# Performance work log

Hardware: AMD Instinct MI355X
Metric: run time of the kernel (lower is better)

Reference implementation:

```python
import jax, jax.numpy as jnp
import numpy as np

N = 100000
E = 1600000
IN_DIM = 128
OUT_DIM = 64


def setup_inputs() -> dict:
    key = jax.random.key(0)
    k_h, k_ei, k_ew, k_W, k_a = jax.random.split(key, 5)
    h = jax.random.normal(k_h, (N, IN_DIM), dtype=jnp.float32)
    edge_index = jax.random.randint(k_ei, (2, E), 0, N, dtype=jnp.int64)
    edge_weight = jax.random.uniform(k_ew, (E,), dtype=jnp.float32)
    # nn.Linear weights (Kaiming-uniform-ish scale)
    W = jax.random.uniform(k_W, (OUT_DIM, IN_DIM), dtype=jnp.float32,
                           minval=-1.0, maxval=1.0) / np.sqrt(IN_DIM)
    a = jax.random.uniform(k_a, (2 * OUT_DIM,), dtype=jnp.float32,
                           minval=-1.0, maxval=1.0) / np.sqrt(2 * OUT_DIM)
    return {"h": h, "edge_index": edge_index, "edge_weight": edge_weight,
            "W": W, "a": a}


def reference(h, edge_index, edge_weight, W, a):
    # Faithful translation of _GATConvSparse.forward (inference; dropout = identity).
    n = h.shape[0]
    src, dst = edge_index[0], edge_index[1]
    Wh = h @ W.T                                  # (N, out_dim)
    d = Wh.shape[1]
    # a(cat([Wh[src], Wh[dst]])) == Wh[src] @ a[:d] + Wh[dst] @ a[d:]
    alpha = Wh[src] @ a[:d] + Wh[dst] @ a[d:]     # (E,)
    alpha = alpha * edge_weight
    # Buggy-but-faithful 'softmax': segment-sum raw scores onto dst nodes...
    alpha_node = jax.ops.segment_sum(alpha, dst, num_segments=n)   # (N,)
    alpha_exp = jnp.exp(alpha_node - alpha_node.max())             # (N,)
    # ...then normalize per-edge exp(src) by sum of exp(src) over each dst segment.
    denom = jax.ops.segment_sum(alpha_exp[src], dst, num_segments=n)  # (N,)
    alpha_norm = alpha_exp[src] / (denom[dst] + 1e-9)              # (E,)
    out = jax.ops.segment_sum(alpha_norm[:, None] * Wh[src], dst,
                              num_segments=n)                      # (N, out_dim)
    return jax.nn.elu(out)
```

## Files before the change

kernel.cpp:

```cpp
#include <hip/hip_runtime.h>
#include <math.h>

#define Nn 100000
#define Ee 1600000
#define IND 128
#define OUTD 64
#define DPB 64
#define NB 1563
#define BSTR 1536
#define CAP 1536
#define GB 1563
#define EB_BLOCKS 391
#define AGG_BLOCKS 1024
#define AFIX 1048576.0f

using bf16x8 = __attribute__((ext_vector_type(8))) short;
using f32x4 = __attribute__((ext_vector_type(4))) float;

__device__ __forceinline__ unsigned short f2bf(float f) {
    unsigned u = __float_as_uint(f);
    u = u + 0x7FFFu + ((u >> 16) & 1u);
    return (unsigned short)(u >> 16);
}
__device__ __forceinline__ float bf2f(unsigned short h) {
    return __uint_as_float(((unsigned)h) << 16);
}

__device__ __forceinline__ bool probe64(const void* __restrict__ ei) {
    const long long* p = (const long long*)ei;
    bool ok = true;
#pragma unroll
    for (int i = 0; i < 8; ++i) {
        long long v = p[i];
        ok = ok && (v >= 0 && v < Nn);
    }
    return ok;
}

__device__ __forceinline__ void load_edge(const void* ei, int e, bool is64,
                                          int& s, int& d) {
    if (is64) {
        const long long* p = (const long long*)ei;
        s = (int)p[e];
        d = (int)p[Ee + e];
    } else {
        const int* p = (const int*)ei;
        s = p[e];
        d = p[Ee + e];
    }
}

__global__ __launch_bounds__(256) void k_fused(
    const float* __restrict__ h, const float* __restrict__ W,
    const float* __restrict__ a, unsigned short* __restrict__ Whb,
    float* __restrict__ s1, float* __restrict__ s2) {
    __shared__ unsigned short Ash[64][136];
    __shared__ unsigned short Wsh[64][136];
    __shared__ float al[2 * OUTD];
    int bid = blockIdx.x;
    int t = threadIdx.x;

    int R = bid * 64;
    for (int i = t; i < 2048; i += 256) {
        float4 v = ((const float4*)W)[i];
        int r = i >> 5, c = (i & 31) << 2;
        unsigned lo = (unsigned)f2bf(v.x) | ((unsigned)f2bf(v.y) << 16);
        unsigned hi = (unsigned)f2bf(v.z) | ((unsigned)f2bf(v.w) << 16);
        *(uint2*)&Wsh[r][c] = make_uint2(lo, hi);
    }
    if (t < 32) ((float4*)al)[t] = ((const float4*)a)[t];
    for (int i = t; i < 2048; i += 256) {
        int r = i >> 5, c = (i & 31) << 2;
        int n = R + r;
        float4 v = make_float4(0.f, 0.f, 0.f, 0.f);
        if (n < Nn) v = ((const float4*)(h + (size_t)n * IND))[i & 31];
        unsigned lo = (unsigned)f2bf(v.x) | ((unsigned)f2bf(v.y) << 16);
        unsigned hi = (unsigned)f2bf(v.z) | ((unsigned)f2bf(v.w) << 16);
        *(uint2*)&Ash[r][c] = make_uint2(lo, hi);
    }
    __syncthreads();

    int w = t >> 6, l = t & 63;
    int li = l & 15, lg = l >> 4;
    f32x4 acc[4];
#pragma unroll
    for (int nt = 0; nt < 4; ++nt) acc[nt] = (f32x4){0.f, 0.f, 0.f, 0.f};
#pragma unroll
    for (int kk = 0; kk < 4; ++kk) {
        bf16x8 af = *(const bf16x8*)&Ash[w * 16 + li][kk * 32 + lg * 8];
#pragma unroll
        for (int nt = 0; nt < 4; ++nt) {
            bf16x8 bf = *(const bf16x8*)&Wsh[nt * 16 + li][kk * 32 + lg * 8];
            acc[nt] = __builtin_amdgcn_mfma_f32_16x16x32_bf16(af, bf,
                                                              acc[nt],
                                                              0, 0, 0);
        }
    }
    float p1[4] = {0.f, 0.f, 0.f, 0.f};
    float p2[4] = {0.f, 0.f, 0.f, 0.f};
#pragma unroll
    for (int nt = 0; nt < 4; ++nt) {
        float a1v = al[nt * 16 + li];
        float a2v = al[OUTD + nt * 16 + li];
#pragma unroll
        for (int r = 0; r < 4; ++r) {
            float v = acc[nt][r];
            p1[r] += v * a1v;
            p2[r] += v * a2v;
            int row = R + w * 16 + lg * 4 + r;
            if (row < Nn)
                Whb[(size_t)row * OUTD + nt * 16 + li] = f2bf(v);
        }
    }
#pragma unroll
    for (int r = 0; r < 4; ++r) {
#pragma unroll
        for (int m = 1; m < 16; m <<= 1) {
            p1[r] += __shfl_xor(p1[r], m, 64);
            p2[r] += __shfl_xor(p2[r], m, 64);
        }
    }
    if (li < 4) {
        int row = R + w * 16 + lg * 4 + li;
        if (row < Nn) {
            s1[row] = p1[li];
            s2[row] = p2[li];
        }
    }
}

__global__ __launch_bounds__(512) void k_binscatter(
    const void* __restrict__ ei, const float* __restrict__ ew,
    const float* __restrict__ s1, const float* __restrict__ s2,
    int* __restrict__ bcursor, uint2* __restrict__ bins) {
    __shared__ int cnt[NB];
    __shared__ int gbase[NB];
    for (int i = threadIdx.x; i < NB; i += 512) cnt[i] = 0;
    __syncthreads();
    bool is64 = probe64(ei);
    int base = blockIdx.x * 4096;
    unsigned rx[8];
    int ryi[8];
    int rb[8];
    int rk[8];
#pragma unroll
    for (int i = 0; i < 8; ++i) {
        int e = base + i * 512 + threadIdx.x;
        rb[i] = -1;
        rx[i] = 0;
        ryi[i] = 0;
        rk[i] = 0;
        if (e < Ee) {
            int s, d;
            load_edge(ei, e, is64, s, d);
            float alpha = (s1[s] + s2[d]) * ew[e];
            ryi[i] = (int)rintf(alpha * AFIX);
            int b = d >> 6;
            rb[i] = b;
            rk[i] = atomicAdd(&cnt[b], 1);
            rx[i] = ((unsigned)s << 7) | ((unsigned)(d & 63) << 24);
        }
    }
    __syncthreads();
    for (int i = threadIdx.x; i < NB; i += 512) {
        int c = cnt[i];
        if (c) gbase[i] = atomicAdd(bcursor + i, c);
    }
    __syncthreads();
#pragma unroll
    for (int i = 0; i < 8; ++i) {
        if (rb[i] >= 0) {
            int pos = gbase[rb[i]] + rk[i];
            if (pos < BSTR)
                bins[(size_t)rb[i] * BSTR + pos] =
                    make_uint2(rx[i], (unsigned)ryi[i]);
        }
    }
}

__global__ __launch_bounds__(256) void k_balpha(
    const uint2* __restrict__ bins, const int* __restrict__ bcnt,
    float* __restrict__ ae) {
    __shared__ int anl[DPB];
    int b = blockIdx.x;
    int t = threadIdx.x;
    if (t < DPB) anl[t] = 0;
    __syncthreads();
    int e0 = b * BSTR;
    int c = bcnt[b];
    int e1 = e0 + (c < BSTR ? c : BSTR);
    for (int k = e0 + t; k < e1; k += 256) {
        uint2 r = bins[k];
        atomicAdd(&anl[r.x >> 24], (int)r.y);
    }
    __syncthreads();
    if (t < DPB) {
        int n = b * DPB + t;
        if (n < Nn) ae[n] = expf((float)anl[t] * (1.f / AFIX));
    }
}

#define AGG_BODY(NR)                                                         \
    {                                                                        \
        uint2 rr[NR];                                                        \
        uint2 ww[NR];                                                        \
        _Pragma("unroll") for (int j = 0; j < NR; ++j)                       \
            rr[j] = lp[4 * j];                                               \
        _Pragma("unroll") for (int j = 0; j < NR; ++j)                       \
            ww[j] = *(const uint2*)(whbB + (rr[j].x + ql8));                 \
        _Pragma("unroll") for (int j = 0; j < NR; ++j) {                     \
            float aa = __uint_as_float(rr[j].y);                             \
            acc.x += aa * __uint_as_float(ww[j].x << 16);                    \
            acc.y += aa * __uint_as_float(ww[j].x & 0xFFFF0000u);            \
            acc.z += aa * __uint_as_float(ww[j].y << 16);                    \
            acc.w += aa * __uint_as_float(ww[j].y & 0xFFFF0000u);            \
            den += aa;                                                       \
        }                                                                    \
        lp += 4 * NR;                                                        \
    }

__global__ __launch_bounds__(512, 4) void k_agg(
    const uint2* __restrict__ bins, const int* __restrict__ bcnt,
    const float* __restrict__ ae, const unsigned short* __restrict__ Whb,
    float* __restrict__ out, int* __restrict__ wctr) {
    __shared__ uint2 lrec[CAP];
    __shared__ int cnt[DPB];
    __shared__ int sbase[DPB];
    __shared__ int bsh;
    int t = threadIdx.x;
    int lane = t & 63;
    int wave = t >> 6;
    int q = lane >> 4;
    int ql = lane & 15;
    unsigned ql8 = (unsigned)ql << 3;
    const char* whbB = (const char*)Whb;

    for (;;) {
        if (t == 0) bsh = atomicAdd(wctr, 1);
        if (t < DPB) cnt[t] = 0;
        __syncthreads();
        int b = bsh;
        if (b >= NB) break;
        int e0 = b * BSTR;
        int c = bcnt[b];
        int total = c < BSTR ? c : BSTR;
        int e1 = e0 + total;

        unsigned su[CAP / 512];
        float sa[CAP / 512];
        int srk[CAP / 512];
#pragma unroll
        for (int i = 0; i < CAP / 512; ++i) {
            int k = e0 + i * 512 + t;
            srk[i] = -1;
            if (k < e1) {
                uint2 r = bins[k];
                srk[i] = atomicAdd(&cnt[r.x >> 24], 1);
                su[i] = r.x;
                sa[i] = ae[(r.x >> 7) & 0x1FFFF];
            }
        }
        __syncthreads();
        if (t < DPB) {
            int v = cnt[t];
#pragma unroll
            for (int d = 1; d < DPB; d <<= 1) {
                int u = __shfl_up(v, d, 64);
                if (t >= d) v += u;
            }
            sbase[t] = v;
        }
        __syncthreads();
#pragma unroll
        for (int i = 0; i < CAP / 512; ++i) {
            if (srk[i] >= 0) {
                int dloc = su[i] >> 24;
                int pos = sbase[dloc] - cnt[dloc] + srk[i];
                lrec[pos] = make_uint2(su[i] & 0x00FFFF80u,
                                       __float_as_uint(sa[i]));
            }
        }
        __syncthreads();

        for (int d = wave * 8; d < wave * 8 + 8; ++d) {
            int k1 = sbase[d];
            int k = k1 - cnt[d];
            const uint2* lp = lrec + k + q;
            float4 acc = make_float4(0.f, 0.f, 0.f, 0.f);
            float den = 0.f;
            for (; k + 15 < k1; k += 16) AGG_BODY(4);
            for (; k + 7 < k1; k += 8) AGG_BODY(2);
            for (; k + 3 < k1; k += 4) AGG_BODY(1);
            if (k < k1) {
                int idx = k + q;
                int cl = idx < k1 ? idx : k1 - 1;
                uint2 rA = lrec[cl];
                float aA = idx < k1 ? __uint_as_float(rA.y) : 0.f;
                uint2 wA = *(const uint2*)(whbB + (rA.x + ql8));
                acc.x += aA * __uint_as_float(wA.x << 16);
                acc.y += aA * __uint_as_float(wA.x & 0xFFFF0000u);
                acc.z += aA * __uint_as_float(wA.y << 16);
                acc.w += aA * __uint_as_float(wA.y & 0xFFFF0000u);
                den += aA;
            }
#pragma unroll
            for (int m = 16; m <= 32; m <<= 1) {
                acc.x += __shfl_xor(acc.x, m, 64);
                acc.y += __shfl_xor(acc.y, m, 64);
                acc.z += __shfl_xor(acc.z, m, 64);
                acc.w += __shfl_xor(acc.w, m, 64);
                den += __shfl_xor(den, m, 64);
            }
            if (q == 0) {
                int n = b * DPB + d;
                if (n < Nn) {
                    float inv = 1.f / (den + 1e-9f);
                    float vx = acc.x * inv;
                    float vy = acc.y * inv;
                    float vz = acc.z * inv;
                    float vw = acc.w * inv;
                    vx = vx > 0.f ? vx : expm1f(vx);
                    vy = vy > 0.f ? vy : expm1f(vy);
                    vz = vz > 0.f ? vz : expm1f(vz);
                    vw = vw > 0.f ? vw : expm1f(vw);
                    *(float4*)&out[(size_t)n * OUTD + ql * 4] =
                        make_float4(vx, vy, vz, vw);
                }
            }
        }
        __syncthreads();
    }
}

extern "C" void kernel_launch(void* const* d_in, const int* in_sizes, int n_in,
                              void* d_out, int out_size, void* d_ws,
                              size_t ws_size, hipStream_t stream) {
    const float* h = (const float*)d_in[0];
    const void* ei = d_in[1];
    const float* ew = (const float*)d_in[2];
    const float* W = (const float*)d_in[3];
    const float* a = (const float*)d_in[4];
    float* out = (float*)d_out;

    unsigned short* Whb = (unsigned short*)d_ws;
    float* s1 = (float*)(Whb + (size_t)Nn * OUTD);
    float* s2 = s1 + Nn;
    float* ae = s2 + Nn;
    int* bcursor = (int*)(ae + Nn);
    int* wctr = bcursor + 2048;
    uint2* bins = (uint2*)(wctr + 16);

    hipMemsetAsync(bcursor, 0, (2048 + 16) * sizeof(int), stream);

    k_fused<<<GB, 256, 0, stream>>>(h, W, a, Whb, s1, s2);
    k_binscatter<<<EB_BLOCKS, 512, 0, stream>>>(ei, ew, s1, s2, bcursor, bins);
    k_balpha<<<NB, 256, 0, stream>>>(bins, bcursor, ae);
    k_agg<<<AGG_BLOCKS, 512, 0, stream>>>(bins, bcursor, ae, Whb, out, wctr);
}
```

Measured before the change: 124.5 us.

## Use one block per bin in aggregation and split waves into two 32-lane halves

The aggregation kernel drops its persistent work-stealing loop (atomic work counter, 1024 blocks) and launches one block per dst bin instead. Each wave now processes two edges at a time, with 32 lanes each gathering 4 bytes (two bf16 features) per edge, where before it used four 16-lane quarters gathering 8 bytes each. The cross-lane reduction drops from two shuffle rounds to one, and the workspace counter and its memset go away. In exchange, each edge row is gathered with narrower per-lane loads, and block launch overhead replaces the dynamic scheduling.

```diff
diff --git a/kernel.cpp b/kernel.cpp
--- a/kernel.cpp
+++ b/kernel.cpp
@@ -11,7 +11,6 @@
 #define CAP 1536
 #define GB 1563
 #define EB_BLOCKS 391
-#define AGG_BLOCKS 1024
 #define AFIX 1048576.0f
 
 using bf16x8 = __attribute__((ext_vector_type(8))) short;
@@ -203,132 +202,111 @@
 #define AGG_BODY(NR)                                                         \
     {                                                                        \
         uint2 rr[NR];                                                        \
-        uint2 ww[NR];                                                        \
+        unsigned ww[NR];                                                     \
         _Pragma("unroll") for (int j = 0; j < NR; ++j)                       \
-            rr[j] = lp[4 * j];                                               \
+            rr[j] = lp[2 * j];                                               \
         _Pragma("unroll") for (int j = 0; j < NR; ++j)                       \
-            ww[j] = *(const uint2*)(whbB + (rr[j].x + ql8));                 \
+            ww[j] = *(const unsigned*)(whbB + (rr[j].x + hl4));              \
         _Pragma("unroll") for (int j = 0; j < NR; ++j) {                     \
             float aa = __uint_as_float(rr[j].y);                             \
-            acc.x += aa * __uint_as_float(ww[j].x << 16);                    \
-            acc.y += aa * __uint_as_float(ww[j].x & 0xFFFF0000u);            \
-            acc.z += aa * __uint_as_float(ww[j].y << 16);                    \
-            acc.w += aa * __uint_as_float(ww[j].y & 0xFFFF0000u);            \
+            acc.x += aa * __uint_as_float(ww[j] << 16);                      \
+            acc.y += aa * __uint_as_float(ww[j] & 0xFFFF0000u);              \
             den += aa;                                                       \
         }                                                                    \
-        lp += 4 * NR;                                                        \
+        lp += 2 * NR;                                                        \
     }
 
 __global__ __launch_bounds__(512, 4) void k_agg(
     const uint2* __restrict__ bins, const int* __restrict__ bcnt,
     const float* __restrict__ ae, const unsigned short* __restrict__ Whb,
-    float* __restrict__ out, int* __restrict__ wctr) {
+    float* __restrict__ out) {
     __shared__ uint2 lrec[CAP];
     __shared__ int cnt[DPB];
     __shared__ int sbase[DPB];
-    __shared__ int bsh;
+    int b = blockIdx.x;
     int t = threadIdx.x;
     int lane = t & 63;
     int wave = t >> 6;
-    int q = lane >> 4;
-    int ql = lane & 15;
-    unsigned ql8 = (unsigned)ql << 3;
+    int half = lane >> 5;
+    int hl = lane & 31;
+    unsigned hl4 = (unsigned)hl << 2;
+    int e0 = b * BSTR;
+    int c = bcnt[b];
+    int total = c < BSTR ? c : BSTR;
+    int e1 = e0 + total;
     const char* whbB = (const char*)Whb;
 
-    for (;;) {
-        if (t == 0) bsh = atomicAdd(wctr, 1);
-        if (t < DPB) cnt[t] = 0;
-        __syncthreads();
-        int b = bsh;
-        if (b >= NB) break;
-        int e0 = b * BSTR;
-        int c = bcnt[b];
-        int total = c < BSTR ? c : BSTR;
-        int e1 = e0 + total;
-
-        unsigned su[CAP / 512];
-        float sa[CAP / 512];
-        int srk[CAP / 512];
-#pragma unroll
-        for (int i = 0; i < CAP / 512; ++i) {
-            int k = e0 + i * 512 + t;
-            srk[i] = -1;
-            if (k < e1) {
-                uint2 r = bins[k];
-                srk[i] = atomicAdd(&cnt[r.x >> 24], 1);
-                su[i] = r.x;
-                sa[i] = ae[(r.x >> 7) & 0x1FFFF];
+    if (t < DPB) cnt[t] = 0;
+    __syncthreads();
+
+    unsigned su[CAP / 512];
+    float sa[CAP / 512];
+    int srk[CAP / 512];
+#pragma unroll
+    for (int i = 0; i < CAP / 512; ++i) {
+        int k = e0 + i * 512 + t;
+        srk[i] = -1;
+        if (k < e1) {
+            uint2 r = bins[k];
+            srk[i] = atomicAdd(&cnt[r.x >> 24], 1);
+            su[i] = r.x;
+            sa[i] = ae[(r.x >> 7) & 0x1FFFF];
+        }
+    }
+    __syncthreads();
+    if (t < DPB) {
+        int v = cnt[t];
+#pragma unroll
+        for (int d = 1; d < DPB; d <<= 1) {
+            int u = __shfl_up(v, d, 64);
+            if (t >= d) v += u;
+        }
+        sbase[t] = v;
+    }
+    __syncthreads();
+#pragma unroll
+    for (int i = 0; i < CAP / 512; ++i) {
+        if (srk[i] >= 0) {
+            int dloc = su[i] >> 24;
+            int pos = sbase[dloc] - cnt[dloc] + srk[i];
+            lrec[pos] = make_uint2(su[i] & 0x00FFFF80u,
+                                   __float_as_uint(sa[i]));
+        }
+    }
+    __syncthreads();
+
+    for (int d = wave * 8; d < wave * 8 + 8; ++d) {
+        int k1 = sbase[d];
+        int k = k1 - cnt[d];
+        const uint2* lp = lrec + k + half;
+        float2 acc = make_float2(0.f, 0.f);
+        float den = 0.f;
+        for (; k + 15 < k1; k += 16) AGG_BODY(8);
+        for (; k + 7 < k1; k += 8) AGG_BODY(4);
+        for (; k + 1 < k1; k += 2) AGG_BODY(1);
+        if (k < k1) {
+            uint2 rA = lrec[k];
+            unsigned wA = *(const unsigned*)(whbB + (rA.x + hl4));
+            float aA = half ? 0.f : __uint_as_float(rA.y);
+            acc.x += aA * __uint_as_float(wA << 16);
+            acc.y += aA * __uint_as_float(wA & 0xFFFF0000u);
+            den += aA;
+        }
+        float ax = acc.x + __shfl_xor(acc.x, 32, 64);
+        float ay = acc.y + __shfl_xor(acc.y, 32, 64);
+        float dn = den + __shfl_xor(den, 32, 64);
+        if (half == 0) {
+            int n = b * DPB + d;
+            if (n < Nn) {
+                float inv = 1.f / (dn + 1e-9f);
+                float vx = ax * inv;
+                float vy = ay * inv;
+                vx = vx > 0.f ? vx : expm1f(vx);
+                vy = vy > 0.f ? vy : expm1f(vy);
+                *(float2*)&out[(size_t)n * OUTD + hl * 2] =
+                    make_float2(vx, vy);
             }
         }
-        __syncthreads();
-        if (t < DPB) {
-            int v = cnt[t];
-#pragma unroll
-            for (int d = 1; d < DPB; d <<= 1) {
-                int u = __shfl_up(v, d, 64);
-                if (t >= d) v += u;
-            }
-            sbase[t] = v;
-        }
-        __syncthreads();
-#pragma unroll
-        for (int i = 0; i < CAP / 512; ++i) {
-            if (srk[i] >= 0) {
-                int dloc = su[i] >> 24;
-                int pos = sbase[dloc] - cnt[dloc] + srk[i];
-                lrec[pos] = make_uint2(su[i] & 0x00FFFF80u,
-                                       __float_as_uint(sa[i]));
-            }
-        }
-        __syncthreads();
-
-        for (int d = wave * 8; d < wave * 8 + 8; ++d) {
-            int k1 = sbase[d];
-            int k = k1 - cnt[d];
-            const uint2* lp = lrec + k + q;
-            float4 acc = make_float4(0.f, 0.f, 0.f, 0.f);
-            float den = 0.f;
-            for (; k + 15 < k1; k += 16) AGG_BODY(4);
-            for (; k + 7 < k1; k += 8) AGG_BODY(2);
-            for (; k + 3 < k1; k += 4) AGG_BODY(1);
-            if (k < k1) {
-                int idx = k + q;
-                int cl = idx < k1 ? idx : k1 - 1;
-                uint2 rA = lrec[cl];
-                float aA = idx < k1 ? __uint_as_float(rA.y) : 0.f;
-                uint2 wA = *(const uint2*)(whbB + (rA.x + ql8));
-                acc.x += aA * __uint_as_float(wA.x << 16);
-                acc.y += aA * __uint_as_float(wA.x & 0xFFFF0000u);
-                acc.z += aA * __uint_as_float(wA.y << 16);
-                acc.w += aA * __uint_as_float(wA.y & 0xFFFF0000u);
-                den += aA;
-            }
-#pragma unroll
-            for (int m = 16; m <= 32; m <<= 1) {
-                acc.x += __shfl_xor(acc.x, m, 64);
-                acc.y += __shfl_xor(acc.y, m, 64);
-                acc.z += __shfl_xor(acc.z, m, 64);
-                acc.w += __shfl_xor(acc.w, m, 64);
-                den += __shfl_xor(den, m, 64);
-            }
-            if (q == 0) {
-                int n = b * DPB + d;
-                if (n < Nn) {
-                    float inv = 1.f / (den + 1e-9f);
-                    float vx = acc.x * inv;
-                    float vy = acc.y * inv;
-                    float vz = acc.z * inv;
-                    float vw = acc.w * inv;
-                    vx = vx > 0.f ? vx : expm1f(vx);
-                    vy = vy > 0.f ? vy : expm1f(vy);
-                    vz = vz > 0.f ? vz : expm1f(vz);
-                    vw = vw > 0.f ? vw : expm1f(vw);
-                    *(float4*)&out[(size_t)n * OUTD + ql * 4] =
-                        make_float4(vx, vy, vz, vw);
-                }
-            }
-        }
-        __syncthreads();
     }
 }
 
@@ -347,13 +325,12 @@
     float* s2 = s1 + Nn;
     float* ae = s2 + Nn;
     int* bcursor = (int*)(ae + Nn);
-    int* wctr = bcursor + 2048;
-    uint2* bins = (uint2*)(wctr + 16);
-
-    hipMemsetAsync(bcursor, 0, (2048 + 16) * sizeof(int), stream);
+    uint2* bins = (uint2*)(bcursor + 2048);
+
+    hipMemsetAsync(bcursor, 0, 2048 * sizeof(int), stream);
 
     k_fused<<<GB, 256, 0, stream>>>(h, W, a, Whb, s1, s2);
     k_binscatter<<<EB_BLOCKS, 512, 0, stream>>>(ei, ew, s1, s2, bcursor, bins);
     k_balpha<<<NB, 256, 0, stream>>>(bins, bcursor, ae);
-    k_agg<<<AGG_BLOCKS, 512, 0, stream>>>(bins, bcursor, ae, Whb, out, wctr);
-}
+    k_agg<<<NB, 512, 0, stream>>>(bins, bcursor, ae, Whb, out);
+}
```

After: 107.6 us. 13.5% less time.
